# Performance work log

Measured on AMD Instinct MI355X. Metric: run time of the kernel, lower is better.

Reference implementation:

```python
import jax, jax.numpy as jnp
import numpy as np

EPS = 1e-8


def setup_inputs() -> dict:
    key = jax.random.key(0)
    ks = jax.random.split(key, 4)
    B, Cin, Cout, K, S, H, W = 16, 256, 256, 3, 512, 128, 128
    return {
        "x": jax.random.normal(ks[0], (B, Cin, H, W), dtype=jnp.float32),
        "style": jax.random.normal(ks[1], (B, S), dtype=jnp.float32),
        "weight": jax.random.normal(ks[2], (1, Cout, Cin, K, K), dtype=jnp.float32),
        "mod_w": jax.random.normal(ks[3], (Cin, S), dtype=jnp.float32) * (1.0 / np.sqrt(S)),
        "mod_b": jnp.zeros((Cin,), dtype=jnp.float32),
        "bias": jnp.zeros((1, Cout, 1, 1), dtype=jnp.float32),
    }


def reference(x, style, weight, mod_w, mod_b, bias):
    B, Cin, H, W = x.shape
    _, Cout, _, K, _ = weight.shape
    scale = 1.0 / np.sqrt(Cin * K * K)

    # modulation: Linear(style_dim -> in_channel)
    s = style @ mod_w.T + mod_b                      # [B, Cin]
    w = scale * weight * s[:, None, :, None, None]   # [B, Cout, Cin, K, K]
    demod = jax.lax.rsqrt(jnp.sum(w * w, axis=(2, 3, 4)) + EPS)  # [B, Cout]
    w = w * demod[:, :, None, None, None]

    # grouped conv with groups = batch (per-sample weights)
    w = w.reshape(B * Cout, Cin, K, K)
    xg = x.reshape(1, B * Cin, H, W)
    out = jax.lax.conv_general_dilated(
        xg, w,
        window_strides=(1, 1),
        padding=[(1, 1), (1, 1)],
        dimension_numbers=("NCHW", "OIHW", "NCHW"),
        feature_group_count=B,
    )
    Ho, Wo = out.shape[2], out.shape[3]
    out = out.reshape(B, Cout, Ho, Wo)
    return out + bias
```

## Files before the change

kernel.cpp:

```cpp
#include <hip/hip_runtime.h>
#include <stdint.h>

typedef unsigned short u16;
typedef __attribute__((ext_vector_type(8))) short short8;
typedef __attribute__((ext_vector_type(4))) float f32x4;

#define AS1 __attribute__((address_space(1)))
#define AS3 __attribute__((address_space(3)))

static __device__ __forceinline__ void gload_lds16(const void* g, void* l) {
  __builtin_amdgcn_global_load_lds((const AS1 void*)g, (AS3 void*)l, 16, 0, 0);
}

static __device__ __forceinline__ u16 bf16r(float f) {
  union { float f; uint32_t u; } c; c.f = f;
  uint32_t u = c.u;
  u += 0x7fffu + ((u >> 16) & 1u);
  return (u16)(u >> 16);
}

static constexpr int NB = 16, CIN = 256, COUT = 256, HW = 128, SDIM = 512;
static constexpr float SCALE = 1.0f / 48.0f;

__global__ void k_style(const float* __restrict__ style, const float* __restrict__ mod_w,
                        const float* __restrict__ mod_b, float* __restrict__ s) {
  int b = blockIdx.x, ci = threadIdx.x;
  const float4* st = (const float4*)(style + (size_t)b * SDIM);
  const float4* mw = (const float4*)(mod_w + (size_t)ci * SDIM);
  float acc = 0.f;
  #pragma unroll 4
  for (int j = 0; j < SDIM / 4; ++j) {
    float4 a = st[j], w = mw[j];
    acc += a.x * w.x + a.y * w.y + a.z * w.z + a.w * w.w;
  }
  s[b * CIN + ci] = acc + mod_b[ci];
}

__global__ void k_wmod(const float* __restrict__ weight, const float* __restrict__ s,
                       u16* __restrict__ Wb) {
  __shared__ float wld[CIN * 9];
  __shared__ float red[8];
  int bid = blockIdx.x;
  int b = bid >> 8, co = bid & 255;
  int t = threadIdx.x;
  const float* wsrc = weight + (size_t)co * (CIN * 9);
  for (int i = t; i < CIN * 9; i += 256) wld[i] = wsrc[i];
  __syncthreads();
  int ci = t;
  float sv = s[b * CIN + ci];
  float v[9];
  float sq = 0.f;
  #pragma unroll
  for (int k = 0; k < 9; ++k) {
    float w = SCALE * wld[ci * 9 + k] * sv;
    v[k] = w;
    sq += w * w;
  }
  #pragma unroll
  for (int off = 32; off; off >>= 1) sq += __shfl_down(sq, off);
  int lane = t & 63, wid = t >> 6;
  if (lane == 0) red[wid] = sq;
  __syncthreads();
  if (t == 0) red[4] = rsqrtf(red[0] + red[1] + red[2] + red[3] + 1e-8f);
  __syncthreads();
  float demod = red[4];
  #pragma unroll
  for (int k = 0; k < 9; ++k) {
    Wb[(((size_t)b * 9 + k) * COUT + co) * CIN + ci] = bf16r(v[k] * demod);
  }
}

__global__ void k_xt(const float* __restrict__ x, u16* __restrict__ xTp) {
  __shared__ u16 T[128 * 65];
  int bid = blockIdx.x;
  int b = bid >> 7, h = bid & 127;
  int t = threadIdx.x;
  size_t rowbase = ((size_t)b * 130 + (h + 1)) * 130 * CIN;
  xTp[rowbase + t] = 0;
  xTp[rowbase + (size_t)129 * CIN + t] = 0;
  if (h == 0) {
    uint32_t* g = (uint32_t*)(xTp + (size_t)b * 130 * 130 * CIN);
    for (int i = t; i < 130 * CIN / 2; i += 256) g[i] = 0;
  }
  if (h == 127) {
    uint32_t* g = (uint32_t*)(xTp + ((size_t)b * 130 + 129) * 130 * CIN);
    for (int i = t; i < 130 * CIN / 2; i += 256) g[i] = 0;
  }
  for (int ci0 = 0; ci0 < CIN; ci0 += 64) {
    __syncthreads();
    #pragma unroll
    for (int i = 0; i < 8; ++i) {
      int idx = t + i * 256;
      int ci = idx >> 5, px4 = idx & 31;
      float4 v = *(const float4*)(x + (((size_t)b * CIN + ci0 + ci) * HW + h) * HW + px4 * 4);
      T[(px4 * 4 + 0) * 65 + ci] = bf16r(v.x);
      T[(px4 * 4 + 1) * 65 + ci] = bf16r(v.y);
      T[(px4 * 4 + 2) * 65 + ci] = bf16r(v.z);
      T[(px4 * 4 + 3) * 65 + ci] = bf16r(v.w);
    }
    __syncthreads();
    int ci = t & 63, pxo = t >> 6;
    #pragma unroll
    for (int i = 0; i < 32; ++i) {
      int px = i * 4 + pxo;
      xTp[rowbase + (size_t)(px + 1) * CIN + ci0 + ci] = T[px * 65 + ci];
    }
  }
}

static constexpr int SLOTU = 32768;

__global__ __launch_bounds__(512, 2) void k_conv(const u16* __restrict__ Wb,
                                                 const u16* __restrict__ xTp,
                                                 const float* __restrict__ bias,
                                                 float* __restrict__ out) {
  extern __shared__ u16 lds[];
  int bid = blockIdx.x;
  int swz = (bid & 7) * 128 + (bid >> 3);
  int b = swz >> 6, hp = swz & 63;
  int h0 = hp * 2;

  int t = threadIdx.x, lane = t & 63, wid = t >> 6;
  int wr = wid >> 2, wc = wid & 3;
  int rowoff = wid * 8 + (lane >> 3);
  int swzc = ((lane & 7) ^ (lane >> 3)) << 3;
  int cxor = (lane & 7) << 3;
  int klo = (lane >> 4) << 3;
  int arow = (wr * 128 + (lane & 15)) * 64;
  int brow = (wc * 64 + (lane & 15)) * 64;
  const size_t wbB = (size_t)b * 9 * 65536;
  const size_t xB = (size_t)b * 130 * 130 * 256;

  f32x4 acc[8][4];
  #pragma unroll
  for (int i = 0; i < 8; ++i)
    #pragma unroll
    for (int j = 0; j < 4; ++j) acc[i][j] = (f32x4)0.f;

  auto srcA = [&](int kta, int i) -> const u16* {
    int kpos = kta >> 2, ci0 = (kta & 3) << 6;
    return Wb + wbB + (size_t)kpos * 65536 + (size_t)(i * 64 + rowoff) * 256 + ci0 + swzc;
  };
  auto srcB = [&](int kta, int i) -> const u16* {
    int kpos = kta >> 2, ci0 = (kta & 3) << 6;
    int kh = kpos < 3 ? 0 : (kpos < 6 ? 1 : 2);
    int kw = kpos - kh * 3;
    int hh = h0 + kh + (i >> 1);
    int pxp = kw + (i & 1) * 64 + rowoff;
    return xTp + xB + ((size_t)hh * 130 + pxp) * 256 + ci0 + swzc;
  };

  {
    u16* A2 = lds;
    u16* B2 = lds + 16384;
    #pragma unroll
    for (int i = 0; i < 4; ++i) gload_lds16(srcA(0, i), A2 + (i * 64 + wid * 8) * 64);
    #pragma unroll
    for (int i = 0; i < 4; ++i) gload_lds16(srcB(0, i), B2 + (i * 64 + wid * 8) * 64);
  }
  asm volatile("s_waitcnt vmcnt(0)" ::: "memory");
  __builtin_amdgcn_s_barrier();
  asm volatile("" ::: "memory");

  for (int kt = 0; kt < 36; ++kt) {
    u16* Ac = lds + (kt & 1) * SLOTU;
    u16* Bc = Ac + 16384;
    u16* An = lds + ((kt & 1) ^ 1) * SLOTU;
    u16* Bn = An + 16384;
    bool pf = kt < 35;
    int kta = kt + 1;

    short8 bf[4][2], af0[2], af1[2];

#define LD_A(M, KK) (*(const short8*)&Ac[arow + (M) * 1024 + (((KK) * 32 + klo) ^ cxor)])
#define LD_B(N, KK) (*(const short8*)&Bc[brow + (N) * 1024 + (((KK) * 32 + klo) ^ cxor)])
#define MFMA_PAIR(M)                                                                       \
    _Pragma("unroll")                                                                      \
    for (int nt = 0; nt < 4; ++nt) {                                                       \
      acc[(M)][nt]     = __builtin_amdgcn_mfma_f32_16x16x32_bf16(af0[0], bf[nt][0], acc[(M)][nt], 0, 0, 0);     \
      acc[(M)][nt]     = __builtin_amdgcn_mfma_f32_16x16x32_bf16(af0[1], bf[nt][1], acc[(M)][nt], 0, 0, 0);     \
      acc[(M) + 1][nt] = __builtin_amdgcn_mfma_f32_16x16x32_bf16(af1[0], bf[nt][0], acc[(M) + 1][nt], 0, 0, 0); \
      acc[(M) + 1][nt] = __builtin_amdgcn_mfma_f32_16x16x32_bf16(af1[1], bf[nt][1], acc[(M) + 1][nt], 0, 0, 0); \
    }
#define PHASE_BAR()                        \
    asm volatile("" ::: "memory");         \
    __builtin_amdgcn_s_barrier();          \
    asm volatile("" ::: "memory");

    #pragma unroll
    for (int nt = 0; nt < 4; ++nt) { bf[nt][0] = LD_B(nt, 0); bf[nt][1] = LD_B(nt, 1); }
    af0[0] = LD_A(0, 0); af0[1] = LD_A(0, 1);
    af1[0] = LD_A(1, 0); af1[1] = LD_A(1, 1);
    if (pf) {
      #pragma unroll
      for (int i = 0; i < 4; ++i) gload_lds16(srcA(kta, i), An + (i * 64 + wid * 8) * 64);
    }
    PHASE_BAR();
    __builtin_amdgcn_s_setprio(1);
    MFMA_PAIR(0);
    __builtin_amdgcn_s_setprio(0);
    PHASE_BAR();
    af0[0] = LD_A(2, 0); af0[1] = LD_A(2, 1);
    af1[0] = LD_A(3, 0); af1[1] = LD_A(3, 1);
    if (pf) {
      #pragma unroll
      for (int i = 0; i < 4; ++i) gload_lds16(srcB(kta, i), Bn + (i * 64 + wid * 8) * 64);
    }
    PHASE_BAR();
    __builtin_amdgcn_s_setprio(1);
    MFMA_PAIR(2);
    __builtin_amdgcn_s_setprio(0);
    PHASE_BAR();
    af0[0] = LD_A(4, 0); af0[1] = LD_A(4, 1);
    af1[0] = LD_A(5, 0); af1[1] = LD_A(5, 1);
    PHASE_BAR();
    __builtin_amdgcn_s_setprio(1);
    MFMA_PAIR(4);
    __builtin_amdgcn_s_setprio(0);
    PHASE_BAR();
    af0[0] = LD_A(6, 0); af0[1] = LD_A(6, 1);
    af1[0] = LD_A(7, 0); af1[1] = LD_A(7, 1);
    PHASE_BAR();
    __builtin_amdgcn_s_setprio(1);
    MFMA_PAIR(6);
    __builtin_amdgcn_s_setprio(0);
    PHASE_BAR();
    if (pf) asm volatile("s_waitcnt vmcnt(0)" ::: "memory");
    __builtin_amdgcn_s_barrier();
    asm volatile("" ::: "memory");
#undef LD_A
#undef LD_B
#undef MFMA_PAIR
#undef PHASE_BAR
  }

  #pragma unroll
  for (int mt = 0; mt < 8; ++mt) {
    #pragma unroll
    for (int j = 0; j < 4; ++j) {
      int co = wr * 128 + mt * 16 + ((lane >> 4) * 4) + j;
      float bv = bias[co];
      #pragma unroll
      for (int nt = 0; nt < 4; ++nt) {
        int px = wc * 64 + nt * 16 + (lane & 15);
        int h = h0 + (px >> 7), w = px & 127;
        out[(((size_t)b * COUT + co) * HW + h) * HW + w] = acc[mt][nt][j] + bv;
      }
    }
  }
}

extern "C" void kernel_launch(void* const* d_in, const int* in_sizes, int n_in,
                              void* d_out, int out_size, void* d_ws, size_t ws_size,
                              hipStream_t stream) {
  const float* x      = (const float*)d_in[0];
  const float* style  = (const float*)d_in[1];
  const float* weight = (const float*)d_in[2];
  const float* mod_w  = (const float*)d_in[3];
  const float* mod_b  = (const float*)d_in[4];
  const float* bias   = (const float*)d_in[5];
  float* out = (float*)d_out;

  char* ws = (char*)d_ws;
  float* s   = (float*)ws;
  u16* Wb    = (u16*)(ws + 16384);
  u16* xTp   = (u16*)(ws + 16384 + (size_t)NB * 9 * COUT * CIN * 2);

  (void)hipFuncSetAttribute((const void*)k_conv,
                            hipFuncAttributeMaxDynamicSharedMemorySize, 2 * SLOTU * 2);

  k_style<<<NB, 256, 0, stream>>>(style, mod_w, mod_b, s);
  k_wmod<<<NB * COUT, 256, 0, stream>>>(weight, s, Wb);
  k_xt<<<NB * HW, 256, 0, stream>>>(x, xTp);
  k_conv<<<NB * (HW / 2), 512, 2 * SLOTU * 2, stream>>>(Wb, xTp, bias, out);
}
```

Baseline: 411.8 us.

## Restructure conv K-loop into two k-half phases with fewer barriers, occupancy 1

Replaces the four M-pair phases per K tile, which had eight barriers, with two phases split by k-half. Each phase loads all 8 A and 4 B fragments and then issues 32 MFMAs back to back. This cuts barrier count and LDS fragment reloads. Launch bounds drop to one block per CU, giving more registers per thread, at the cost of losing the second resident block that could hide latency.

```diff
diff --git a/kernel.cpp b/kernel.cpp
--- a/kernel.cpp
+++ b/kernel.cpp
@@ -110,7 +110,7 @@
 
 static constexpr int SLOTU = 32768;
 
-__global__ __launch_bounds__(512, 2) void k_conv(const u16* __restrict__ Wb,
+__global__ __launch_bounds__(512, 1) void k_conv(const u16* __restrict__ Wb,
                                                  const u16* __restrict__ xTp,
                                                  const float* __restrict__ bias,
                                                  float* __restrict__ out) {
@@ -170,68 +170,57 @@
     bool pf = kt < 35;
     int kta = kt + 1;
 
-    short8 bf[4][2], af0[2], af1[2];
+    short8 af[8], bf[4];
 
 #define LD_A(M, KK) (*(const short8*)&Ac[arow + (M) * 1024 + (((KK) * 32 + klo) ^ cxor)])
 #define LD_B(N, KK) (*(const short8*)&Bc[brow + (N) * 1024 + (((KK) * 32 + klo) ^ cxor)])
-#define MFMA_PAIR(M)                                                                       \
-    _Pragma("unroll")                                                                      \
-    for (int nt = 0; nt < 4; ++nt) {                                                       \
-      acc[(M)][nt]     = __builtin_amdgcn_mfma_f32_16x16x32_bf16(af0[0], bf[nt][0], acc[(M)][nt], 0, 0, 0);     \
-      acc[(M)][nt]     = __builtin_amdgcn_mfma_f32_16x16x32_bf16(af0[1], bf[nt][1], acc[(M)][nt], 0, 0, 0);     \
-      acc[(M) + 1][nt] = __builtin_amdgcn_mfma_f32_16x16x32_bf16(af1[0], bf[nt][0], acc[(M) + 1][nt], 0, 0, 0); \
-      acc[(M) + 1][nt] = __builtin_amdgcn_mfma_f32_16x16x32_bf16(af1[1], bf[nt][1], acc[(M) + 1][nt], 0, 0, 0); \
-    }
-#define PHASE_BAR()                        \
-    asm volatile("" ::: "memory");         \
-    __builtin_amdgcn_s_barrier();          \
-    asm volatile("" ::: "memory");
-
-    #pragma unroll
-    for (int nt = 0; nt < 4; ++nt) { bf[nt][0] = LD_B(nt, 0); bf[nt][1] = LD_B(nt, 1); }
-    af0[0] = LD_A(0, 0); af0[1] = LD_A(0, 1);
-    af1[0] = LD_A(1, 0); af1[1] = LD_A(1, 1);
+
+    #pragma unroll
+    for (int mt = 0; mt < 8; ++mt) af[mt] = LD_A(mt, 0);
+    #pragma unroll
+    for (int nt = 0; nt < 4; ++nt) bf[nt] = LD_B(nt, 0);
     if (pf) {
       #pragma unroll
       for (int i = 0; i < 4; ++i) gload_lds16(srcA(kta, i), An + (i * 64 + wid * 8) * 64);
     }
-    PHASE_BAR();
+    asm volatile("" ::: "memory");
+    __builtin_amdgcn_s_barrier();
+    asm volatile("" ::: "memory");
     __builtin_amdgcn_s_setprio(1);
-    MFMA_PAIR(0);
+    #pragma unroll
+    for (int mt = 0; mt < 8; ++mt)
+      #pragma unroll
+      for (int nt = 0; nt < 4; ++nt)
+        acc[mt][nt] = __builtin_amdgcn_mfma_f32_16x16x32_bf16(af[mt], bf[nt], acc[mt][nt], 0, 0, 0);
     __builtin_amdgcn_s_setprio(0);
-    PHASE_BAR();
-    af0[0] = LD_A(2, 0); af0[1] = LD_A(2, 1);
-    af1[0] = LD_A(3, 0); af1[1] = LD_A(3, 1);
+    asm volatile("" ::: "memory");
+    __builtin_amdgcn_s_barrier();
+    asm volatile("" ::: "memory");
+
+    #pragma unroll
+    for (int mt = 0; mt < 8; ++mt) af[mt] = LD_A(mt, 1);
+    #pragma unroll
+    for (int nt = 0; nt < 4; ++nt) bf[nt] = LD_B(nt, 1);
     if (pf) {
       #pragma unroll
       for (int i = 0; i < 4; ++i) gload_lds16(srcB(kta, i), Bn + (i * 64 + wid * 8) * 64);
     }
-    PHASE_BAR();
+    asm volatile("" ::: "memory");
+    __builtin_amdgcn_s_barrier();
+    asm volatile("" ::: "memory");
     __builtin_amdgcn_s_setprio(1);
-    MFMA_PAIR(2);
+    #pragma unroll
+    for (int mt = 0; mt < 8; ++mt)
+      #pragma unroll
+      for (int nt = 0; nt < 4; ++nt)
+        acc[mt][nt] = __builtin_amdgcn_mfma_f32_16x16x32_bf16(af[mt], bf[nt], acc[mt][nt], 0, 0, 0);
     __builtin_amdgcn_s_setprio(0);
-    PHASE_BAR();
-    af0[0] = LD_A(4, 0); af0[1] = LD_A(4, 1);
-    af1[0] = LD_A(5, 0); af1[1] = LD_A(5, 1);
-    PHASE_BAR();
-    __builtin_amdgcn_s_setprio(1);
-    MFMA_PAIR(4);
-    __builtin_amdgcn_s_setprio(0);
-    PHASE_BAR();
-    af0[0] = LD_A(6, 0); af0[1] = LD_A(6, 1);
-    af1[0] = LD_A(7, 0); af1[1] = LD_A(7, 1);
-    PHASE_BAR();
-    __builtin_amdgcn_s_setprio(1);
-    MFMA_PAIR(6);
-    __builtin_amdgcn_s_setprio(0);
-    PHASE_BAR();
     if (pf) asm volatile("s_waitcnt vmcnt(0)" ::: "memory");
+    asm volatile("" ::: "memory");
     __builtin_amdgcn_s_barrier();
     asm volatile("" ::: "memory");
 #undef LD_A
 #undef LD_B
-#undef MFMA_PAIR
-#undef PHASE_BAR
   }
 
   #pragma unroll
```

Result: no change. 413.2 us (+0.3%).
